# Kernel tuning notes

Measured on AMD Instinct MI355X. Metric: run time of the kernel, lower is better.

## Reference

```python
import jax, jax.numpy as jnp
import numpy as np

N, NUM_TOKENS, TOKEN_DIM = 32768, 8192, 768
K = 4  # hard-coded top-k in the torch forward


def setup_inputs() -> dict:
    key = jax.random.key(0)
    k1, k2 = jax.random.split(key)
    inputs_flatten = jax.random.normal(k1, (N, TOKEN_DIM), dtype=jnp.float32)
    embed = jax.random.normal(k2, (NUM_TOKENS, TOKEN_DIM), dtype=jnp.float32)  # codebook buffer
    return {"inputs_flatten": inputs_flatten, "embed": embed}


def reference(inputs_flatten, embed):
    # squared euclidean distances: [N, num_tokens]
    distances = (
        jnp.sum(inputs_flatten ** 2, axis=1, keepdims=True)
        + jnp.sum(embed ** 2, axis=1)
        - 2.0 * (inputs_flatten @ embed.T)
    )

    # k smallest distances via top_k on negated distances
    neg_vals, topk_indices = jax.lax.top_k(-distances, K)
    topk_values = -neg_vals  # ascending smallest-k distances, [N, 4]

    # drop nearest, reweight the next 3 neighbors
    tv = topk_values[:, 1:]  # [N, 3]
    tv = tv / jnp.maximum(jnp.linalg.norm(tv, axis=1, keepdims=True), 1e-12)  # F.normalize
    tv = 1.0 / (tv + 1e-4)
    topk_values = jax.nn.softmax(tv, axis=1)
    topk_indices_out = topk_indices[:, 1:]

    # hard assignment (argmin) and codebook lookup (one-hot scatter + matmul == gather)
    encoding_indices = jnp.argmin(distances, axis=1)[:, None]  # [N, 1]
    quantize = embed[encoding_indices[:, 0]]  # [N, token_dim]

    # straight-through estimator
    quantize = jax.lax.stop_gradient(quantize - inputs_flatten) + inputs_flatten
    return quantize, encoding_indices, topk_values, topk_indices_out
```

## Files before the change

kernel.cpp:

```cpp
#include <hip/hip_runtime.h>
#include <cfloat>
#include <cmath>

#define NROWS 32768
#define NTOK  8192
#define DIM   768
#define KSPLIT 384

#define BM 64
#define BN 128
#define BK 32
#define NT 512

#define Q_OFF   0
#define EI_OFF  (NROWS*DIM)
#define TV_OFF  (EI_OFF + NROWS)
#define TI_OFF  (TV_OFF + NROWS*3)

typedef short short8 __attribute__((ext_vector_type(8)));
typedef float f32x4 __attribute__((ext_vector_type(4)));
typedef float f32x16 __attribute__((ext_vector_type(16)));

__global__ __launch_bounds__(256)
void np_norm_kernel(const float* __restrict__ x, float* __restrict__ o) {
#pragma clang fp contract(off)
  const int wid = (blockIdx.x * 256 + threadIdx.x) >> 6;
  const int lane = threadIdx.x & 63;
  const float* p = x + (size_t)wid * DIM + (lane >> 3) * 96 + (lane & 7);
  float v = p[0];
  float r = v * v;
#pragma unroll
  for (int k = 1; k < 12; k++) {
    float w = p[8 * k];
    float sq = w * w;
    r = r + sq;
  }
#pragma unroll
  for (int m = 1; m < 64; m <<= 1) {
    float other = __shfl_xor(r, m, 64);
    r = r + other;
  }
  if (lane == 0) o[wid] = r;
}

__device__ __forceinline__ bool dless(float a, int ai, float b, int bi_) {
  return (a < b) || (a == b && ai < bi_);
}

__device__ __forceinline__ void ins4(float (&v)[4], int (&x)[4], float c, int ci) {
  if (dless(c, ci, v[3], x[3])) {
    v[3] = c; x[3] = ci;
    if (dless(v[3], x[3], v[2], x[2])) { float tv = v[2]; int ti = x[2]; v[2] = v[3]; x[2] = x[3]; v[3] = tv; x[3] = ti; }
    if (dless(v[2], x[2], v[1], x[1])) { float tv = v[1]; int ti = x[1]; v[1] = v[2]; x[1] = x[2]; v[2] = tv; x[2] = ti; }
    if (dless(v[1], x[1], v[0], x[0])) { float tv = v[0]; int ti = x[0]; v[0] = v[1]; x[0] = x[1]; v[1] = tv; x[1] = ti; }
  }
}

__device__ __forceinline__ void ins8(float (&v)[8], int (&x)[8], float c, int ci) {
  if (dless(c, ci, v[7], x[7])) {
    v[7] = c; x[7] = ci;
#pragma unroll
    for (int k = 7; k > 0; k--) {
      if (dless(v[k], x[k], v[k - 1], x[k - 1])) {
        float tv = v[k - 1]; int ti = x[k - 1];
        v[k - 1] = v[k]; x[k - 1] = x[k];
        v[k] = tv; x[k] = ti;
      }
    }
  }
}

__device__ __forceinline__ void ins8v(float (&v)[8], int (&x)[8], float c, int ci) {
  v[7] = c; x[7] = ci;
#pragma unroll
  for (int k = 7; k > 0; k--) {
    const bool sw = v[k] < v[k - 1];
    const float vmin = fminf(v[k], v[k - 1]);
    const float vmax = fmaxf(v[k], v[k - 1]);
    const int xk1 = sw ? x[k] : x[k - 1];
    const int xk  = sw ? x[k - 1] : x[k];
    v[k - 1] = vmin; v[k] = vmax;
    x[k - 1] = xk1;  x[k] = xk;
  }
}

__device__ __forceinline__ unsigned short f2bf(float f) {
  unsigned int u = __float_as_uint(f);
  u += 0x7FFFu + ((u >> 16) & 1u);
  return (unsigned short)(u >> 16);
}

typedef const __attribute__((address_space(1))) void* gas1_t;
typedef __attribute__((address_space(3))) void* las3_t;
__device__ __forceinline__ void gl16(const void* g, void* s) {
  __builtin_amdgcn_global_load_lds((gas1_t)g, (las3_t)s, 16, 0, 0);
}

__global__ __launch_bounds__(256)
void cvtT_kernel(const float* __restrict__ in, unsigned short* __restrict__ out, int nrows) {
  const int row = blockIdx.x * 256 + threadIdx.x;
  const int Q = blockIdx.y;
  const float4* p = (const float4*)(in + (size_t)row * DIM + Q * 8);
  const float4 a = p[0], b = p[1];
  union { unsigned short u[8]; int4 v; } pk;
  pk.u[0] = f2bf(a.x); pk.u[1] = f2bf(a.y); pk.u[2] = f2bf(a.z); pk.u[3] = f2bf(a.w);
  pk.u[4] = f2bf(b.x); pk.u[5] = f2bf(b.y); pk.u[6] = f2bf(b.z); pk.u[7] = f2bf(b.w);
  *(int4*)(out + ((size_t)Q * nrows + row) * 8) = pk.v;
}

#define STRIPS 16
#define KSTEPS 24
#define NITER (STRIPS * KSTEPS)

__global__ __launch_bounds__(256, 2)
void vq_rank(const unsigned short* __restrict__ xbT, const unsigned short* __restrict__ ebT,
             const float* __restrict__ e2g, unsigned short* __restrict__ topp) {
  __shared__ __align__(16) unsigned char esm[4][16384];

  const int tid = threadIdx.x;
  const int l = tid & 63;
  const int w = tid >> 6;
  const int wr = w >> 1, wc = w & 1;
  const int l31 = l & 31, h = l >> 5;

  const int bid = (int)blockIdx.x;
  const int sbid = (bid & 7) * 64 + (bid >> 3);
  const int chalf = sbid >> 8;
  const int row0 = (sbid & 255) * 128;
  const int cg0 = chalf * 4096;

  const size_t xinv0 = ((size_t)h * NROWS + row0 + wr * 64 + l31) * 8;
  const size_t xinv1 = xinv0 + 32 * 8;

  float bv[2][8]; int bi[2][8];
#pragma unroll
  for (int xj = 0; xj < 2; ++xj)
#pragma unroll
    for (int c = 0; c < 8; ++c) { bv[xj][c] = FLT_MAX; bi[xj][c] = 0x7FFFFFFF; }

  f32x16 acc[4][2];
#pragma unroll
  for (int ei = 0; ei < 4; ++ei)
#pragma unroll
    for (int xj = 0; xj < 2; ++xj) acc[ei][xj] = (f32x16)0.f;

  short8 xb0[4], xb1[4];

#define STAGE_E(BN_, KT, COL0)                                                  \
  {                                                                             \
    const unsigned short* eg = ebT + ((size_t)(4 * (KT)) * NTOK + (COL0) + tid) * 8; \
    gl16(eg,                &esm[BN_][(0 * 256 + w * 64) * 16]);                \
    gl16(eg + NTOK * 8,     &esm[BN_][(1 * 256 + w * 64) * 16]);                \
    gl16(eg + 2 * NTOK * 8, &esm[BN_][(2 * 256 + w * 64) * 16]);                \
    gl16(eg + 3 * NTOK * 8, &esm[BN_][(3 * 256 + w * 64) * 16]);                \
  }

#define XLOAD(XB, KT)                                                           \
  {                                                                             \
    const unsigned short* xp = xbT + (size_t)(4 * (KT)) * (NROWS * 8);          \
    XB[0] = *(const short8*)(xp + xinv0);                                       \
    XB[1] = *(const short8*)(xp + xinv1);                                       \
    XB[2] = *(const short8*)(xp + 2 * NROWS * 8 + xinv0);                       \
    XB[3] = *(const short8*)(xp + 2 * NROWS * 8 + xinv1);                       \
  }

#define COMPUTE(B_, XB)                                                         \
  {                                                                             \
    const unsigned char* ebp = &esm[B_][0];                                     \
    __builtin_amdgcn_s_setprio(1);                                              \
    _Pragma("unroll")                                                           \
    for (int s = 0; s < 2; ++s) {                                               \
      const int kq = s * 2 + h;                                                 \
      short8 af[4];                                                             \
      _Pragma("unroll")                                                         \
      for (int ei = 0; ei < 4; ++ei)                                            \
        af[ei] = *(const short8*)(ebp + (size_t)(kq * 256 + wc * 128 + ei * 32 + l31) * 16); \
      _Pragma("unroll")                                                         \
      for (int ei = 0; ei < 4; ++ei)                                            \
        _Pragma("unroll")                                                       \
        for (int xj = 0; xj < 2; ++xj)                                          \
          acc[ei][xj] = __builtin_amdgcn_mfma_f32_32x32x16_bf16(af[ei], XB[s * 2 + xj], acc[ei][xj], 0, 0, 0); \
    }                                                                           \
    __builtin_amdgcn_s_setprio(0);                                              \
  }

#define SELECT(SC0)                                                             \
  {                                                                             \
    _Pragma("unroll")                                                           \
    for (int ei = 0; ei < 4; ++ei) {                                            \
      const int cb = (SC0) + wc * 128 + ei * 32 + 4 * h;                        \
      float4 e2q[4];                                                            \
      _Pragma("unroll")                                                         \
      for (int q = 0; q < 4; ++q)                                               \
        e2q[q] = *(const float4*)(e2g + cb + q * 8);                            \
      _Pragma("unroll")                                                         \
      for (int xj = 0; xj < 2; ++xj) {                                          \
        _Pragma("unroll")                                                       \
        for (int q = 0; q < 4; ++q) {                                           \
          const float c0 = fmaf(-2.f, acc[ei][xj][q * 4 + 0], e2q[q].x);        \
          const float c1 = fmaf(-2.f, acc[ei][xj][q * 4 + 1], e2q[q].y);        \
          const float c2 = fmaf(-2.f, acc[ei][xj][q * 4 + 2], e2q[q].z);        \
          const float c3 = fmaf(-2.f, acc[ei][xj][q * 4 + 3], e2q[q].w);        \
          if (c0 < bv[xj][7]) ins8v(bv[xj], bi[xj], c0, cb + q * 8 + 0);        \
          if (c1 < bv[xj][7]) ins8v(bv[xj], bi[xj], c1, cb + q * 8 + 1);        \
          if (c2 < bv[xj][7]) ins8v(bv[xj], bi[xj], c2, cb + q * 8 + 2);        \
          if (c3 < bv[xj][7]) ins8v(bv[xj], bi[xj], c3, cb + q * 8 + 3);        \
        }                                                                       \
      }                                                                         \
    }                                                                           \
    _Pragma("unroll")                                                           \
    for (int ei = 0; ei < 4; ++ei)                                              \
      _Pragma("unroll")                                                         \
      for (int xj = 0; xj < 2; ++xj) acc[ei][xj] = (f32x16)0.f;                 \
  }

#define BODY(B_, XB, DO_X, DO_S, WAITS)                                         \
  {                                                                             \
    asm volatile(WAITS ::: "memory");                                           \
    __builtin_amdgcn_s_barrier();                                               \
    asm volatile("" ::: "memory");                                              \
    COMPUTE(B_, XB)                                                             \
    if (DO_X) { XLOAD(XB, xkt) if (++xkt == KSTEPS) xkt = 0; }                  \
    if (DO_S) {                                                                 \
      STAGE_E((B_ + 3) & 3, nkt, ncol0)                                         \
      if (++nkt == KSTEPS) { nkt = 0; ncol0 += 256; }                           \
    }                                                                           \
    if (++kc == KSTEPS) { SELECT(scol0) kc = 0; scol0 += 256; }                 \
  }

  STAGE_E(0, 0, cg0)
  XLOAD(xb0, 0)
  STAGE_E(1, 1, cg0)
  XLOAD(xb1, 1)
  STAGE_E(2, 2, cg0)

  int xkt = 2;
  int nkt = 3, ncol0 = cg0;
  int kc = 0, scol0 = cg0;

#pragma unroll 1
  for (int g = 0; g < 95; ++g) {
    BODY(0, xb0, 1, 1, "s_waitcnt vmcnt(12)")
    BODY(1, xb1, 1, 1, "s_waitcnt vmcnt(12)")
    BODY(2, xb0, 1, 1, "s_waitcnt vmcnt(12)")
    BODY(3, xb1, 1, 1, "s_waitcnt vmcnt(12)")
  }
  BODY(0, xb0, 1, 1, "s_waitcnt vmcnt(12)")
  BODY(1, xb1, 1, 0, "s_waitcnt vmcnt(12)")
  BODY(2, xb0, 0, 0, "s_waitcnt vmcnt(8)")
  BODY(3, xb1, 0, 0, "s_waitcnt vmcnt(0)")
#undef BODY
#undef SELECT
#undef COMPUTE
#undef XLOAD
#undef STAGE_E

#pragma unroll
  for (int xj = 0; xj < 2; ++xj) {
    float ov[8]; int oi[8];
#pragma unroll
    for (int c = 0; c < 8; ++c) {
      ov[c] = __shfl_xor(bv[xj][c], 32, 64);
      oi[c] = __shfl_xor(bi[xj][c], 32, 64);
    }
#pragma unroll
    for (int c = 0; c < 8; ++c) ins8(bv[xj], bi[xj], ov[c], oi[c]);
  }

  __syncthreads();
  float* mval = (float*)&esm[0][0];
  int*   midx = (int*)&esm[1][0];
  if (wc == 1 && l < 32) {
#pragma unroll
    for (int xj = 0; xj < 2; ++xj) {
      const int rr = wr * 64 + xj * 32 + l31;
#pragma unroll
      for (int c = 0; c < 8; ++c) {
        mval[rr * 8 + c] = bv[xj][c];
        midx[rr * 8 + c] = bi[xj][c];
      }
    }
  }
  __syncthreads();
  if (wc == 0 && l < 32) {
#pragma unroll
    for (int xj = 0; xj < 2; ++xj) {
      const int rr = wr * 64 + xj * 32 + l31;
#pragma unroll
      for (int c = 0; c < 8; ++c) ins8(bv[xj], bi[xj], mval[rr * 8 + c], midx[rr * 8 + c]);
      unsigned short* dst = topp + (size_t)(row0 + rr) * 16 + chalf * 8;
#pragma unroll
      for (int c = 0; c < 8; ++c) dst[c] = (unsigned short)bi[xj][c];
    }
  }
}

__global__ __launch_bounds__(256)
void vq_refine16(const float* __restrict__ x, const float* __restrict__ E,
                 const float* __restrict__ x2, const float* __restrict__ e2,
                 const unsigned short* __restrict__ topp, float* __restrict__ out) {
  const int gid = blockIdx.x * 256 + threadIdx.x;
  const int row = gid >> 4;
  const int s = gid & 15;
  const int myc = topp[(size_t)row * 16 + s];

  const float4* xr = (const float4*)(x + (size_t)row * DIM);
  const float4* er = (const float4*)(E + (size_t)myc * DIM);
  float accA = 0.f, accB = 0.f;
#pragma unroll 8
  for (int q = 0; q < KSPLIT / 4; ++q) {
    const float4 a = xr[q], b = er[q];
    accA = fmaf(a.x, b.x, accA); accA = fmaf(a.y, b.y, accA);
    accA = fmaf(a.z, b.z, accA); accA = fmaf(a.w, b.w, accA);
  }
#pragma unroll 8
  for (int q = KSPLIT / 4; q < DIM / 4; ++q) {
    const float4 a = xr[q], b = er[q];
    accB = fmaf(a.x, b.x, accB); accB = fmaf(a.y, b.y, accB);
    accB = fmaf(a.z, b.z, accB); accB = fmaf(a.w, b.w, accB);
  }
  const float d = fmaf(-2.0f, accA + accB, x2[row] + e2[myc]);

  const int base = (threadIdx.x & 63) & ~15;
  float dv[16]; int cv[16];
#pragma unroll
  for (int t = 0; t < 16; ++t) {
    dv[t] = __shfl(d, base + t, 64);
    cv[t] = __shfl(myc, base + t, 64);
  }
#pragma unroll
  for (int a = 0; a < 4; ++a)
#pragma unroll
    for (int b = 15; b > a; --b) {
      const bool sw = (dv[b] < dv[b - 1]) || (dv[b] == dv[b - 1] && cv[b] < cv[b - 1]);
      if (sw) {
        float td = dv[b]; dv[b] = dv[b - 1]; dv[b - 1] = td;
        int ti = cv[b]; cv[b] = cv[b - 1]; cv[b - 1] = ti;
      }
    }

  if (s == 0) {
    out[EI_OFF + row] = (float)cv[0];
    const double d1 = (double)dv[1], d2 = (double)dv[2], d3 = (double)dv[3];
    double nrm = sqrt(d1 * d1 + d2 * d2 + d3 * d3);
    nrm = fmax(nrm, 1e-12);
    const double t1 = 1.0 / (d1 / nrm + 1e-4);
    const double t2 = 1.0 / (d2 / nrm + 1e-4);
    const double t3 = 1.0 / (d3 / nrm + 1e-4);
    const double mx = fmax(t1, fmax(t2, t3));
    const double e1 = exp(t1 - mx), e2x = exp(t2 - mx), e3 = exp(t3 - mx);
    const double sm = e1 + e2x + e3;
    out[TV_OFF + row * 3 + 0] = (float)(e1 / sm);
    out[TV_OFF + row * 3 + 1] = (float)(e2x / sm);
    out[TV_OFF + row * 3 + 2] = (float)(e3 / sm);
    out[TI_OFF + row * 3 + 0] = (float)cv[1];
    out[TI_OFF + row * 3 + 1] = (float)cv[2];
    out[TI_OFF + row * 3 + 2] = (float)cv[3];
  }

  const float4* src = (const float4*)(E + (size_t)cv[0] * DIM);
  float4* dst = (float4*)(out + Q_OFF + (size_t)row * DIM);
#pragma unroll
  for (int k = 0; k < 12; ++k) dst[s + k * 16] = src[s + k * 16];
}

__global__ __launch_bounds__(NT, 4)
void vq_main(const float* __restrict__ A, const float* __restrict__ E,
             const float* __restrict__ x2, const float* __restrict__ e2,
             float* __restrict__ out) {
  __shared__ float a_s[BK][BM + 4];
  __shared__ float b_s[BK][BN + 4];

  const int tid = threadIdx.x;
  const int tx = tid & 15;
  const int ty = tid >> 4;
  const int row0 = blockIdx.x * BM;

  const float x2r[2] = { x2[row0 + ty * 2 + 0], x2[row0 + ty * 2 + 1] };

  float bv[2][4];
  int   bi[2][4];
#pragma unroll
  for (int i = 0; i < 2; i++)
#pragma unroll
    for (int c = 0; c < 4; c++) { bv[i][c] = FLT_MAX; bi[i][c] = 0x7FFFFFFF; }

#define GEMM_STEP(k0, ACC)                                                       \
    {                                                                            \
      __syncthreads();                                                           \
      {                                                                          \
        const int r = tid >> 3, kq = tid & 7;                                    \
        const float4 v = *(const float4*)(A + (size_t)(row0 + r) * DIM + (k0 + kq * 4)); \
        a_s[kq * 4 + 0][r] = v.x; a_s[kq * 4 + 1][r] = v.y;                      \
        a_s[kq * 4 + 2][r] = v.z; a_s[kq * 4 + 3][r] = v.w;                      \
        _Pragma("unroll")                                                        \
        for (int s = 0; s < 2; s++) {                                            \
          const int fi = tid + s * NT;                                           \
          const int rb = fi >> 3, kb = fi & 7;                                   \
          const float4 w = *(const float4*)(E + (size_t)(col0 + rb) * DIM + (k0 + kb * 4)); \
          b_s[kb * 4 + 0][rb] = w.x; b_s[kb * 4 + 1][rb] = w.y;                  \
          b_s[kb * 4 + 2][rb] = w.z; b_s[kb * 4 + 3][rb] = w.w;                  \
        }                                                                        \
      }                                                                          \
      __syncthreads();                                                           \
      _Pragma("unroll")                                                          \
      for (int k = 0; k < BK; k++) {                                             \
        const float2 a2 = *(const float2*)&a_s[k][ty * 2];                       \
        float br[8];                                                             \
        *(float4*)(br)     = *(const float4*)&b_s[k][tx * 8];                    \
        *(float4*)(br + 4) = *(const float4*)&b_s[k][tx * 8 + 4];                \
        _Pragma("unroll")                                                        \
        for (int j = 0; j < 8; j++) {                                            \
          ACC[0][j] = fmaf(a2.x, br[j], ACC[0][j]);                              \
          ACC[1][j] = fmaf(a2.y, br[j], ACC[1][j]);                              \
        }                                                                        \
      }                                                                          \
    }

  for (int ct = 0; ct < NTOK / BN; ++ct) {
    const int col0 = ct * BN;

    float accA[2][8], accB[2][8];
#pragma unroll
    for (int i = 0; i < 2; i++)
#pragma unroll
      for (int j = 0; j < 8; j++) { accA[i][j] = 0.f; accB[i][j] = 0.f; }

    for (int k0 = 0; k0 < KSPLIT; k0 += BK) GEMM_STEP(k0, accA)
    for (int k0 = KSPLIT; k0 < DIM; k0 += BK) GEMM_STEP(k0, accB)

    float e2v[8];
    *(float4*)(e2v)     = *(const float4*)(e2 + col0 + tx * 8);
    *(float4*)(e2v + 4) = *(const float4*)(e2 + col0 + tx * 8 + 4);
#pragma unroll
    for (int i = 0; i < 2; i++) {
#pragma unroll
      for (int j = 0; j < 8; j++) {
        const float dot = accA[i][j] + accB[i][j];
        const float se = x2r[i] + e2v[j];
        const float d = fmaf(-2.0f, dot, se);
        const int ci = col0 + tx * 8 + j;
        ins4(bv[i], bi[i], d, ci);
      }
    }
  }
#undef GEMM_STEP

#pragma unroll
  for (int m = 1; m < 16; m <<= 1) {
#pragma unroll
    for (int i = 0; i < 2; i++) {
      float ov[4]; int oi[4];
#pragma unroll
      for (int c = 0; c < 4; c++) {
        ov[c] = __shfl_xor(bv[i][c], m, 64);
        oi[c] = __shfl_xor(bi[i][c], m, 64);
      }
#pragma unroll
      for (int c = 0; c < 4; c++) ins4(bv[i], bi[i], ov[c], oi[c]);
    }
  }

#pragma unroll
  for (int i = 0; i < 2; i++) {
    if (tx == i) {
      const int gr = row0 + ty * 2 + i;
      out[EI_OFF + gr] = (float)bi[i][0];
      const double d1 = (double)bv[i][1], d2 = (double)bv[i][2], d3 = (double)bv[i][3];
      double nrm = sqrt(d1 * d1 + d2 * d2 + d3 * d3);
      nrm = fmax(nrm, 1e-12);
      const double t1 = 1.0 / (d1 / nrm + 1e-4);
      const double t2 = 1.0 / (d2 / nrm + 1e-4);
      const double t3 = 1.0 / (d3 / nrm + 1e-4);
      const double mx = fmax(t1, fmax(t2, t3));
      const double e1 = exp(t1 - mx), e2x = exp(t2 - mx), e3 = exp(t3 - mx);
      const double s = e1 + e2x + e3;
      out[TV_OFF + gr * 3 + 0] = (float)(e1 / s);
      out[TV_OFF + gr * 3 + 1] = (float)(e2x / s);
      out[TV_OFF + gr * 3 + 2] = (float)(e3 / s);
      out[TI_OFF + gr * 3 + 0] = (float)bi[i][1];
      out[TI_OFF + gr * 3 + 1] = (float)bi[i][2];
      out[TI_OFF + gr * 3 + 2] = (float)bi[i][3];
    }
  }

  __syncthreads();
  int* idx_sh = (int*)&a_s[0][0];
  if (tx == 0) idx_sh[ty * 2 + 0] = bi[0][0];
  if (tx == 1) idx_sh[ty * 2 + 1] = bi[1][0];
  __syncthreads();

  for (int f = tid; f < BM * (DIM / 4); f += NT) {
    const int r = f / (DIM / 4);
    const int c = f % (DIM / 4);
    const int e = idx_sh[r];
    const float4 v = *(const float4*)(E + (size_t)e * DIM + c * 4);
    *(float4*)(out + Q_OFF + (size_t)(row0 + r) * DIM + c * 4) = v;
  }
}

extern "C" void kernel_launch(void* const* d_in, const int* in_sizes, int n_in,
                              void* d_out, int out_size, void* d_ws, size_t ws_size,
                              hipStream_t stream) {
  const float* x = (const float*)d_in[0];
  const float* E = (const float*)d_in[1];
  float* out = (float*)d_out;

  unsigned char* ws = (unsigned char*)d_ws;
  float* e2 = (float*)ws;
  float* x2 = (float*)(ws + 32768);
  unsigned short* topp = (unsigned short*)(ws + 32768 + 131072);
  unsigned short* xbT = (unsigned short*)(ws + 32768 + 131072 + 1048576);
  unsigned short* ebT = xbT + (size_t)NROWS * DIM;
  const size_t need = 32768 + 131072 + 1048576 +
                      (size_t)NROWS * DIM * 2 + (size_t)NTOK * DIM * 2;

  np_norm_kernel<<<NTOK / 4, 256, 0, stream>>>(E, e2);
  np_norm_kernel<<<NROWS / 4, 256, 0, stream>>>(x, x2);

  if (ws_size >= need) {
    cvtT_kernel<<<dim3(NROWS / 256, DIM / 8), 256, 0, stream>>>(x, xbT, NROWS);
    cvtT_kernel<<<dim3(NTOK / 256, DIM / 8), 256, 0, stream>>>(E, ebT, NTOK);
    vq_rank<<<512, 256, 0, stream>>>(xbT, ebT, e2, topp);
    vq_refine16<<<NROWS * 16 / 256, 256, 0, stream>>>(x, E, x2, e2, topp, out);
  } else {
    vq_main<<<NROWS / BM, NT, 0, stream>>>(x, E, x2, e2, out);
  }
}
```

Before: 926.3 us.

## Split rank MFMA step into two LDS phases and tile the bf16 transpose

The main rank loop now splits each k-step into two halves. Each half loads its A fragments from LDS, then waits on a barrier and lgkmcnt before issuing its MFMAs with raised priority. The X register prefetch moves after the compute, and the vmcnt thresholds are retuned so more global loads stay in flight. Separately, the fp32→bf16 transpose kernel now stages a 32x32 tile through shared memory so both reads and writes are coalesced. The extra barriers per step cost some synchronisation in exchange for more orderly LDS/MFMA phasing.

```diff
diff --git a/kernel.cpp b/kernel.cpp
--- a/kernel.cpp
+++ b/kernel.cpp
@@ -98,14 +98,28 @@
 
 __global__ __launch_bounds__(256)
 void cvtT_kernel(const float* __restrict__ in, unsigned short* __restrict__ out, int nrows) {
-  const int row = blockIdx.x * 256 + threadIdx.x;
-  const int Q = blockIdx.y;
-  const float4* p = (const float4*)(in + (size_t)row * DIM + Q * 8);
-  const float4 a = p[0], b = p[1];
-  union { unsigned short u[8]; int4 v; } pk;
-  pk.u[0] = f2bf(a.x); pk.u[1] = f2bf(a.y); pk.u[2] = f2bf(a.z); pk.u[3] = f2bf(a.w);
-  pk.u[4] = f2bf(b.x); pk.u[5] = f2bf(b.y); pk.u[6] = f2bf(b.z); pk.u[7] = f2bf(b.w);
-  *(int4*)(out + ((size_t)Q * nrows + row) * 8) = pk.v;
+  __shared__ int4 tile[32][33];
+  const int r0 = blockIdx.x * 32;
+  const int Q0 = blockIdx.y * 32;
+  const int t = threadIdx.x;
+#pragma unroll
+  for (int i = 0; i < 4; ++i) {
+    const int f = t + i * 256;
+    const int qi = f & 31, ri = f >> 5;
+    const float4* p = (const float4*)(in + (size_t)(r0 + ri) * DIM + (Q0 + qi) * 8);
+    const float4 a = p[0], b = p[1];
+    union { unsigned short u[8]; int4 v; } pk;
+    pk.u[0] = f2bf(a.x); pk.u[1] = f2bf(a.y); pk.u[2] = f2bf(a.z); pk.u[3] = f2bf(a.w);
+    pk.u[4] = f2bf(b.x); pk.u[5] = f2bf(b.y); pk.u[6] = f2bf(b.z); pk.u[7] = f2bf(b.w);
+    tile[qi][ri] = pk.v;
+  }
+  __syncthreads();
+#pragma unroll
+  for (int i = 0; i < 4; ++i) {
+    const int f = t + i * 256;
+    const int ri = f & 31, qi = f >> 5;
+    *(int4*)(out + ((size_t)(Q0 + qi) * nrows + r0 + ri) * 8) = tile[qi][ri];
+  }
 }
 
 #define STRIPS 16
@@ -162,26 +176,6 @@
     XB[1] = *(const short8*)(xp + xinv1);                                       \
     XB[2] = *(const short8*)(xp + 2 * NROWS * 8 + xinv0);                       \
     XB[3] = *(const short8*)(xp + 2 * NROWS * 8 + xinv1);                       \
-  }
-
-#define COMPUTE(B_, XB)                                                         \
-  {                                                                             \
-    const unsigned char* ebp = &esm[B_][0];                                     \
-    __builtin_amdgcn_s_setprio(1);                                              \
-    _Pragma("unroll")                                                           \
-    for (int s = 0; s < 2; ++s) {                                               \
-      const int kq = s * 2 + h;                                                 \
-      short8 af[4];                                                             \
-      _Pragma("unroll")                                                         \
-      for (int ei = 0; ei < 4; ++ei)                                            \
-        af[ei] = *(const short8*)(ebp + (size_t)(kq * 256 + wc * 128 + ei * 32 + l31) * 16); \
-      _Pragma("unroll")                                                         \
-      for (int ei = 0; ei < 4; ++ei)                                            \
-        _Pragma("unroll")                                                       \
-        for (int xj = 0; xj < 2; ++xj)                                          \
-          acc[ei][xj] = __builtin_amdgcn_mfma_f32_32x32x16_bf16(af[ei], XB[s * 2 + xj], acc[ei][xj], 0, 0, 0); \
-    }                                                                           \
-    __builtin_amdgcn_s_setprio(0);                                              \
   }
 
 #define SELECT(SC0)                                                             \
@@ -219,12 +213,41 @@
     asm volatile(WAITS ::: "memory");                                           \
     __builtin_amdgcn_s_barrier();                                               \
     asm volatile("" ::: "memory");                                              \
-    COMPUTE(B_, XB)                                                             \
-    if (DO_X) { XLOAD(XB, xkt) if (++xkt == KSTEPS) xkt = 0; }                  \
+    const unsigned char* ebp = &esm[B_][0];                                     \
+    short8 afA[4];                                                              \
+    _Pragma("unroll")                                                           \
+    for (int ei = 0; ei < 4; ++ei)                                              \
+      afA[ei] = *(const short8*)(ebp + (size_t)(h * 256 + wc * 128 + ei * 32 + l31) * 16); \
     if (DO_S) {                                                                 \
       STAGE_E((B_ + 3) & 3, nkt, ncol0)                                         \
       if (++nkt == KSTEPS) { nkt = 0; ncol0 += 256; }                           \
     }                                                                           \
+    __builtin_amdgcn_s_barrier();                                               \
+    asm volatile("s_waitcnt lgkmcnt(0)" ::: "memory");                          \
+    __builtin_amdgcn_sched_barrier(0);                                          \
+    __builtin_amdgcn_s_setprio(1);                                              \
+    _Pragma("unroll")                                                           \
+    for (int ei = 0; ei < 4; ++ei) {                                            \
+      acc[ei][0] = __builtin_amdgcn_mfma_f32_32x32x16_bf16(afA[ei], XB[0], acc[ei][0], 0, 0, 0); \
+      acc[ei][1] = __builtin_amdgcn_mfma_f32_32x32x16_bf16(afA[ei], XB[1], acc[ei][1], 0, 0, 0); \
+    }                                                                           \
+    __builtin_amdgcn_s_setprio(0);                                              \
+    __builtin_amdgcn_s_barrier();                                               \
+    short8 afB[4];                                                              \
+    _Pragma("unroll")                                                           \
+    for (int ei = 0; ei < 4; ++ei)                                              \
+      afB[ei] = *(const short8*)(ebp + (size_t)((2 + h) * 256 + wc * 128 + ei * 32 + l31) * 16); \
+    __builtin_amdgcn_s_barrier();                                               \
+    asm volatile("s_waitcnt lgkmcnt(0)" ::: "memory");                          \
+    __builtin_amdgcn_sched_barrier(0);                                          \
+    __builtin_amdgcn_s_setprio(1);                                              \
+    _Pragma("unroll")                                                           \
+    for (int ei = 0; ei < 4; ++ei) {                                            \
+      acc[ei][0] = __builtin_amdgcn_mfma_f32_32x32x16_bf16(afB[ei], XB[2], acc[ei][0], 0, 0, 0); \
+      acc[ei][1] = __builtin_amdgcn_mfma_f32_32x32x16_bf16(afB[ei], XB[3], acc[ei][1], 0, 0, 0); \
+    }                                                                           \
+    __builtin_amdgcn_s_setprio(0);                                              \
+    if (DO_X) { XLOAD(XB, xkt) if (++xkt == KSTEPS) xkt = 0; }                  \
     if (++kc == KSTEPS) { SELECT(scol0) kc = 0; scol0 += 256; }                 \
   }
 
@@ -240,18 +263,17 @@
 
 #pragma unroll 1
   for (int g = 0; g < 95; ++g) {
-    BODY(0, xb0, 1, 1, "s_waitcnt vmcnt(12)")
-    BODY(1, xb1, 1, 1, "s_waitcnt vmcnt(12)")
-    BODY(2, xb0, 1, 1, "s_waitcnt vmcnt(12)")
-    BODY(3, xb1, 1, 1, "s_waitcnt vmcnt(12)")
-  }
-  BODY(0, xb0, 1, 1, "s_waitcnt vmcnt(12)")
+    BODY(0, xb0, 1, 1, "s_waitcnt vmcnt(16)")
+    BODY(1, xb1, 1, 1, "s_waitcnt vmcnt(16)")
+    BODY(2, xb0, 1, 1, "s_waitcnt vmcnt(16)")
+    BODY(3, xb1, 1, 1, "s_waitcnt vmcnt(16)")
+  }
+  BODY(0, xb0, 1, 1, "s_waitcnt vmcnt(16)")
   BODY(1, xb1, 1, 0, "s_waitcnt vmcnt(12)")
   BODY(2, xb0, 0, 0, "s_waitcnt vmcnt(8)")
-  BODY(3, xb1, 0, 0, "s_waitcnt vmcnt(0)")
+  BODY(3, xb1, 0, 0, "s_waitcnt vmcnt(4)")
 #undef BODY
 #undef SELECT
-#undef COMPUTE
 #undef XLOAD
 #undef STAGE_E
 
@@ -519,8 +541,8 @@
   np_norm_kernel<<<NROWS / 4, 256, 0, stream>>>(x, x2);
 
   if (ws_size >= need) {
-    cvtT_kernel<<<dim3(NROWS / 256, DIM / 8), 256, 0, stream>>>(x, xbT, NROWS);
-    cvtT_kernel<<<dim3(NTOK / 256, DIM / 8), 256, 0, stream>>>(E, ebT, NTOK);
+    cvtT_kernel<<<dim3(NROWS / 32, 3), 256, 0, stream>>>(x, xbT, NROWS);
+    cvtT_kernel<<<dim3(NTOK / 32, 3), 256, 0, stream>>>(E, ebT, NTOK);
     vq_rank<<<512, 256, 0, stream>>>(xbT, ebT, e2, topp);
     vq_refine16<<<NROWS * 16 / 256, 256, 0, stream>>>(x, E, x2, e2, topp, out);
   } else {
```

Result: no change. 929.5 us (+0.3%).
